# Kernel optimization log

Measured on AMD Instinct MI355X. Metric: run time of the kernel, lower is better.

The kernel has to match this reference:

```python
import jax, jax.numpy as jnp
import numpy as np

HC = 4            # hc_mult
HIDDEN = 4096
SINKHORN_ITERS = 5
HC_EPS = 1e-5
NORM_EPS = 1e-6
B, S = 2, 4096


def setup_inputs() -> dict:
    key = jax.random.key(0)
    k0, k1, k2, k3 = jax.random.split(key, 4)
    mix = (2 + HC) * HC  # 24
    return {
        "hidden_streams": jax.random.normal(k0, (B, S, HC, HIDDEN), dtype=jnp.float32),
        # small init so sigmoid/softmax gates stay in a sane range
        "fn": jax.random.normal(k1, (mix, HC * HIDDEN), dtype=jnp.float32) * 0.01,
        "base": jax.random.normal(k2, (mix,), dtype=jnp.float32),
        "scale": jax.random.normal(k3, (3,), dtype=jnp.float32),
    }


def reference(hidden_streams, fn, base, scale):
    hc = HC
    # flatten streams: [B, S, hc*hidden]
    flat = hidden_streams.reshape(hidden_streams.shape[0], hidden_streams.shape[1], -1).astype(jnp.float32)
    rsqrt = jax.lax.rsqrt(jnp.mean(jnp.square(flat), axis=-1, keepdims=True) + NORM_EPS)
    # packed projection to mix=(2+hc)*hc gate logits, RMS-scaled
    mix = jnp.einsum("bsd,md->bsm", flat, fn.astype(jnp.float32)) * rsqrt
    pre_scale, post_scale, comb_scale = scale[0], scale[1], scale[2]
    pre = jax.nn.sigmoid(mix[..., :hc] * pre_scale + base[:hc]) + HC_EPS
    post = 2.0 * jax.nn.sigmoid(mix[..., hc:2 * hc] * post_scale + base[hc:2 * hc])
    comb_logit = mix[..., 2 * hc:].reshape(*mix.shape[:-1], hc, hc) * comb_scale + base[2 * hc:].reshape(hc, hc)
    comb = jax.nn.softmax(comb_logit, axis=-1) + HC_EPS
    comb = comb / (jnp.sum(comb, axis=-2, keepdims=True) + HC_EPS)
    for _ in range(SINKHORN_ITERS - 1):
        comb = comb / (jnp.sum(comb, axis=-1, keepdims=True) + HC_EPS)
        comb = comb / (jnp.sum(comb, axis=-2, keepdims=True) + HC_EPS)
    return pre, post, comb
```

## Files before the change

### kernel.cpp

```cpp
#include <hip/hip_runtime.h>
#include <hip/hip_bf16.h>
#include <math.h>
#include <stdint.h>

#define HC 4
#define DIM 16384
#define MIXN 24
#define NROWS 8192
#define KSPLIT 32
#define KSL 512
#define NSTEPS 16
#define NSTREAM 16
#define ROWS_PER_STREAM 512
#define NTILES 32
#define NBUF 2
#define THREADS1 512
#define WREC 32
#define HC_EPS 1e-5f
#define NORM_EPS 1e-6f

#define PRE_OFF 0
#define POST_OFF (NROWS * HC)
#define COMB_OFF (2 * NROWS * HC)

typedef float f32x4 __attribute__((ext_vector_type(4)));
typedef float accf4 __attribute__((ext_vector_type(4)));
typedef short bf16x8 __attribute__((ext_vector_type(8)));
typedef short bf16x4 __attribute__((ext_vector_type(4)));

__device__ __forceinline__ short f2bf(float x) {
    union { __hip_bfloat16 h; short s; } u;
    u.h = __float2bfloat16(x);
    return u.s;
}

__global__ __launch_bounds__(THREADS1) void hyper_k1(
    const float* __restrict__ hs,
    const float* __restrict__ fn,
    float* __restrict__ ws)
{
    const int tid  = threadIdx.x;
    const int wave = tid >> 6;
    const int lane = tid & 63;
    const int l15  = lane & 15;
    const int kg   = lane >> 4;
    const int ks     = blockIdx.x & (KSPLIT - 1);
    const int stream = blockIdx.x >> 5;

    __shared__ __align__(16) short s_fn[2][NSTEPS][512];
    __shared__ __align__(16) short s_a[NBUF][NSTEPS][512];
    __shared__ float sC[8][400];

    #pragma unroll 1
    for (int p = 0; p < 4; ++p) {
        const int idx  = p * THREADS1 + tid;
        const int kgf  = idx & 3;
        const int s    = (idx >> 2) & 15;
        const int c    = (idx >> 6) & 15;
        const int tile = idx >> 10;
        const int col  = tile ? (c + 8) : c;
        const float* g = fn + (size_t)col * DIM + ks * KSL + s * 32 + kgf * 8;
        const f32x4 v0 = *(const f32x4*)g;
        const f32x4 v1 = *(const f32x4*)(g + 4);
        bf16x8 b = { f2bf(v0.x), f2bf(v0.y), f2bf(v0.z), f2bf(v0.w),
                     f2bf(v1.x), f2bf(v1.y), f2bf(v1.z), f2bf(v1.w) };
        *(bf16x8*)&s_fn[tile][s][(kgf * 16 + c) * 8] = b;
    }
    __syncthreads();

    const int st_slo = lane >> 3;
    const int st_kg  = (lane >> 1) & 3;
    const int st_e   = (lane & 1) * 4;
    const int sr0 = 2 * wave, sr1 = 2 * wave + 1;

    f32x4 RA0, RA1, RA2, RA3;
    f32x4 RB0, RB1, RB2, RB3;

#define ISSUE(P0, P1, P2, P3, T) do { \
    const float* g0 = hs + (size_t)(stream * ROWS_PER_STREAM + (T) * 16 + sr0) * DIM + ks * KSL; \
    const float* g1 = hs + (size_t)(stream * ROWS_PER_STREAM + (T) * 16 + sr1) * DIM + ks * KSL; \
    P0 = *(const f32x4*)(g0 +   0 + lane * 4); \
    P1 = *(const f32x4*)(g0 + 256 + lane * 4); \
    P2 = *(const f32x4*)(g1 +   0 + lane * 4); \
    P3 = *(const f32x4*)(g1 + 256 + lane * 4); \
} while (0)

#define WR1(BUF, Rj, r, j) do { \
    const int s_ = (j) * 8 + st_slo; \
    int byte_ = ((s_ * 64 + st_kg * 16 + (r)) * 16) + st_e * 2; \
    byte_ ^= ((s_ & 7) << 4); \
    bf16x4 v_ = { f2bf(Rj.x), f2bf(Rj.y), f2bf(Rj.z), f2bf(Rj.w) }; \
    *(bf16x4*)((char*)(&s_a[BUF][0][0]) + byte_) = v_; \
} while (0)

#define WRALL(BUF, P0, P1, P2, P3) do { \
    WR1(BUF, P0, sr0, 0); WR1(BUF, P1, sr0, 1); \
    WR1(BUF, P2, sr1, 0); WR1(BUF, P3, sr1, 1); \
} while (0)

    ISSUE(RA0, RA1, RA2, RA3, 0);
    ISSUE(RB0, RB1, RB2, RB3, 1);
    WRALL(0, RA0, RA1, RA2, RA3);
    ISSUE(RA0, RA1, RA2, RA3, 2);

    int buf = 0;
    #pragma unroll 2
    for (int t = 0; t < NTILES; ++t) {
        asm volatile("s_waitcnt lgkmcnt(0)" ::: "memory");
        __builtin_amdgcn_s_barrier();
        __builtin_amdgcn_sched_barrier(0);

        accf4 acc0 = {0.f, 0.f, 0.f, 0.f};
        accf4 acc1 = {0.f, 0.f, 0.f, 0.f};
        accf4 accS = {0.f, 0.f, 0.f, 0.f};
        #pragma unroll
        for (int i = 0; i < 2; ++i) {
            const int s = wave * 2 + i;
            int ab = ((s * 64 + lane) * 16) ^ ((s & 7) << 4);
            const bf16x8 af = *(const bf16x8*)((const char*)(&s_a[buf][0][0]) + ab);
            const bf16x8 b0 = *(const bf16x8*)&s_fn[0][s][lane * 8];
            const bf16x8 b1 = *(const bf16x8*)&s_fn[1][s][lane * 8];
            acc0 = __builtin_amdgcn_mfma_f32_16x16x32_bf16(af, b0, acc0, 0, 0, 0);
            acc1 = __builtin_amdgcn_mfma_f32_16x16x32_bf16(af, b1, acc1, 0, 0, 0);
            accS = __builtin_amdgcn_mfma_f32_16x16x32_bf16(af, af, accS, 0, 0, 0);
        }

        #pragma unroll
        for (int i = 0; i < 4; ++i)
            sC[wave][(kg * 4 + i) * 25 + l15] = acc0[i];
        if (l15 >= 8) {
            #pragma unroll
            for (int i = 0; i < 4; ++i)
                sC[wave][(kg * 4 + i) * 25 + l15 + 8] = acc1[i];
        }
        #pragma unroll
        for (int i = 0; i < 4; ++i)
            if (l15 == kg * 4 + i) sC[wave][l15 * 25 + 24] = accS[i];

        asm volatile("s_waitcnt lgkmcnt(0)" ::: "memory");
        __builtin_amdgcn_s_barrier();
        __builtin_amdgcn_sched_barrier(0);

        if (tid < 400) {
            const int rr = tid / 25, c = tid % 25;
            const float v = sC[0][tid] + sC[1][tid] + sC[2][tid] + sC[3][tid]
                          + sC[4][tid] + sC[5][tid] + sC[6][tid] + sC[7][tid];
            const int row = stream * ROWS_PER_STREAM + t * 16 + rr;
            ws[((size_t)row * KSPLIT + ks) * WREC + c] = v;
        }

        if (t + 1 < NTILES) {
            const int nbuf = buf ^ 1;
            if ((t & 1) == 0) {
                WRALL(nbuf, RB0, RB1, RB2, RB3);
                if (t + 3 < NTILES) ISSUE(RB0, RB1, RB2, RB3, t + 3);
            } else {
                WRALL(nbuf, RA0, RA1, RA2, RA3);
                if (t + 3 < NTILES) ISSUE(RA0, RA1, RA2, RA3, t + 3);
            }
        }
        buf ^= 1;
    }
#undef ISSUE
#undef WR1
#undef WRALL
}

__global__ __launch_bounds__(256) void hyper_k2(
    const float* __restrict__ ws,
    const float* __restrict__ base,
    const float* __restrict__ scale,
    float* __restrict__ out)
{
    const int tid = threadIdx.x;
    const int row = blockIdx.x * 8 + (tid >> 5);
    const int ks  = tid & 31;

    float v[25];
    const float* w = ws + ((size_t)row * KSPLIT + ks) * WREC;
    #pragma unroll
    for (int c = 0; c < 25; ++c) v[c] = w[c];

    #pragma unroll
    for (int off = 16; off >= 1; off >>= 1)
        #pragma unroll
        for (int c = 0; c < 25; ++c) v[c] += __shfl_xor(v[c], off, 32);

    if (ks != 0) return;

    const float rs = 1.0f / sqrtf(v[24] * (1.0f / (float)DIM) + NORM_EPS);
    const float s0 = scale[0], s1 = scale[1], s2 = scale[2];

    #pragma unroll
    for (int i = 0; i < HC; ++i) {
        const float z = v[i] * rs * s0 + base[i];
        out[PRE_OFF + row * HC + i] = 1.0f / (1.0f + expf(-z)) + HC_EPS;
    }
    #pragma unroll
    for (int i = 0; i < HC; ++i) {
        const float z = v[HC + i] * rs * s1 + base[HC + i];
        out[POST_OFF + row * HC + i] = 2.0f / (1.0f + expf(-z));
    }

    float c[HC][HC];
    #pragma unroll
    for (int i = 0; i < HC; ++i) {
        float l[HC];
        #pragma unroll
        for (int j = 0; j < HC; ++j)
            l[j] = v[2 * HC + i * HC + j] * rs * s2 + base[2 * HC + i * HC + j];
        const float mx = fmaxf(fmaxf(l[0], l[1]), fmaxf(l[2], l[3]));
        float e[HC];
        float sum = 0.0f;
        #pragma unroll
        for (int j = 0; j < HC; ++j) { e[j] = expf(l[j] - mx); sum += e[j]; }
        const float inv = 1.0f / sum;
        #pragma unroll
        for (int j = 0; j < HC; ++j) c[i][j] = e[j] * inv + HC_EPS;
    }
    #pragma unroll
    for (int j = 0; j < HC; ++j) {
        const float cs = c[0][j] + c[1][j] + c[2][j] + c[3][j] + HC_EPS;
        const float inv = 1.0f / cs;
        c[0][j] *= inv; c[1][j] *= inv; c[2][j] *= inv; c[3][j] *= inv;
    }
    #pragma unroll
    for (int it = 0; it < 4; ++it) {
        #pragma unroll
        for (int i = 0; i < HC; ++i) {
            const float rsum = c[i][0] + c[i][1] + c[i][2] + c[i][3] + HC_EPS;
            const float inv = 1.0f / rsum;
            c[i][0] *= inv; c[i][1] *= inv; c[i][2] *= inv; c[i][3] *= inv;
        }
        #pragma unroll
        for (int j = 0; j < HC; ++j) {
            const float cs = c[0][j] + c[1][j] + c[2][j] + c[3][j] + HC_EPS;
            const float inv = 1.0f / cs;
            c[0][j] *= inv; c[1][j] *= inv; c[2][j] *= inv; c[3][j] *= inv;
        }
    }
    #pragma unroll
    for (int i = 0; i < HC; ++i)
        #pragma unroll
        for (int j = 0; j < HC; ++j)
            out[COMB_OFF + row * (HC * HC) + i * HC + j] = c[i][j];
}

extern "C" void kernel_launch(void* const* d_in, const int* in_sizes, int n_in,
                              void* d_out, int out_size, void* d_ws, size_t ws_size,
                              hipStream_t stream) {
    const float* hs    = (const float*)d_in[0];
    const float* fn    = (const float*)d_in[1];
    const float* base  = (const float*)d_in[2];
    const float* scale = (const float*)d_in[3];
    float* out = (float*)d_out;
    float* ws  = (float*)d_ws;

    hyper_k1<<<KSPLIT * NSTREAM, THREADS1, 0, stream>>>(hs, fn, ws);
    hyper_k2<<<NROWS / 8, 256, 0, stream>>>(ws, base, scale, out);
}
```

Baseline: 133.6 us.

## Double-buffer partial-sum scratch to drop one barrier per tile and halve grid

```diff
diff --git a/kernel.cpp b/kernel.cpp
--- a/kernel.cpp
+++ b/kernel.cpp
@@ -10,9 +10,9 @@
 #define KSPLIT 32
 #define KSL 512
 #define NSTEPS 16
-#define NSTREAM 16
-#define ROWS_PER_STREAM 512
-#define NTILES 32
+#define NSTREAM 8
+#define ROWS_PER_STREAM 1024
+#define NTILES 64
 #define NBUF 2
 #define THREADS1 512
 #define WREC 32
@@ -49,7 +49,7 @@
 
     __shared__ __align__(16) short s_fn[2][NSTEPS][512];
     __shared__ __align__(16) short s_a[NBUF][NSTEPS][512];
-    __shared__ float sC[8][400];
+    __shared__ float sC[2][8][400];
 
     #pragma unroll 1
     for (int p = 0; p < 4; ++p) {
@@ -73,6 +73,8 @@
     const int st_e   = (lane & 1) * 4;
     const int sr0 = 2 * wave, sr1 = 2 * wave + 1;
 
+    const int red_rr = tid / 25, red_c = tid % 25;
+
     f32x4 RA0, RA1, RA2, RA3;
     f32x4 RB0, RB1, RB2, RB3;
 
@@ -98,6 +100,18 @@
     WR1(BUF, P2, sr1, 0); WR1(BUF, P3, sr1, 1); \
 } while (0)
 
+#define REDUCE(T) do { \
+    if (tid < 400) { \
+        const int par_ = (T) & 1; \
+        const float v_ = sC[par_][0][tid] + sC[par_][1][tid] \
+                       + sC[par_][2][tid] + sC[par_][3][tid] \
+                       + sC[par_][4][tid] + sC[par_][5][tid] \
+                       + sC[par_][6][tid] + sC[par_][7][tid]; \
+        const int row_ = stream * ROWS_PER_STREAM + (T) * 16 + red_rr; \
+        ws[((size_t)row_ * KSPLIT + ks) * WREC + red_c] = v_; \
+    } \
+} while (0)
+
     ISSUE(RA0, RA1, RA2, RA3, 0);
     ISSUE(RB0, RB1, RB2, RB3, 1);
     WRALL(0, RA0, RA1, RA2, RA3);
@@ -109,6 +123,8 @@
         asm volatile("s_waitcnt lgkmcnt(0)" ::: "memory");
         __builtin_amdgcn_s_barrier();
         __builtin_amdgcn_sched_barrier(0);
+
+        if (t > 0) REDUCE(t - 1);
 
         accf4 acc0 = {0.f, 0.f, 0.f, 0.f};
         accf4 acc1 = {0.f, 0.f, 0.f, 0.f};
@@ -125,28 +141,19 @@
             accS = __builtin_amdgcn_mfma_f32_16x16x32_bf16(af, af, accS, 0, 0, 0);
         }
 
-        #pragma unroll
-        for (int i = 0; i < 4; ++i)
-            sC[wave][(kg * 4 + i) * 25 + l15] = acc0[i];
-        if (l15 >= 8) {
+        {
+            const int par = t & 1;
             #pragma unroll
             for (int i = 0; i < 4; ++i)
-                sC[wave][(kg * 4 + i) * 25 + l15 + 8] = acc1[i];
-        }
-        #pragma unroll
-        for (int i = 0; i < 4; ++i)
-            if (l15 == kg * 4 + i) sC[wave][l15 * 25 + 24] = accS[i];
-
-        asm volatile("s_waitcnt lgkmcnt(0)" ::: "memory");
-        __builtin_amdgcn_s_barrier();
-        __builtin_amdgcn_sched_barrier(0);
-
-        if (tid < 400) {
-            const int rr = tid / 25, c = tid % 25;
-            const float v = sC[0][tid] + sC[1][tid] + sC[2][tid] + sC[3][tid]
-                          + sC[4][tid] + sC[5][tid] + sC[6][tid] + sC[7][tid];
-            const int row = stream * ROWS_PER_STREAM + t * 16 + rr;
-            ws[((size_t)row * KSPLIT + ks) * WREC + c] = v;
+                sC[par][wave][(kg * 4 + i) * 25 + l15] = acc0[i];
+            if (l15 >= 8) {
+                #pragma unroll
+                for (int i = 0; i < 4; ++i)
+                    sC[par][wave][(kg * 4 + i) * 25 + l15 + 8] = acc1[i];
+            }
+            #pragma unroll
+            for (int i = 0; i < 4; ++i)
+                if (l15 == kg * 4 + i) sC[par][wave][l15 * 25 + 24] = accS[i];
         }
 
         if (t + 1 < NTILES) {
@@ -161,9 +168,14 @@
         }
         buf ^= 1;
     }
+
+    asm volatile("s_waitcnt lgkmcnt(0)" ::: "memory");
+    __builtin_amdgcn_s_barrier();
+    REDUCE(NTILES - 1);
 #undef ISSUE
 #undef WR1
 #undef WRALL
+#undef REDUCE
 }
 
 __global__ __launch_bounds__(256) void hyper_k2(
```

After: 127.0 us, median of 2. -5.0%, faster.
